# Kernel optimization log

Hardware: AMD Instinct MI355X
Metric: run time of the kernel (lower is better)

The kernel has to match this reference:

```python
import jax, jax.numpy as jnp
import numpy as np

PERMS = ((0, 1, 2, 3), (2, 1, 3, 0), (3, 1, 0, 2))


def setup_inputs() -> dict:
    key = jax.random.key(0)
    ks = jax.random.split(key, 10)
    N_n1, F = 50000, 128
    N_imp = 100000
    H = 512
    h = jax.random.normal(ks[0], (N_n1, F), dtype=jnp.float32)
    idx = jax.random.randint(ks[1], (N_imp, 4), 0, N_n1, dtype=jnp.int64)
    s = 0.05
    W1 = jax.random.normal(ks[2], (4 * F, H), dtype=jnp.float32) * s
    b1 = jax.random.normal(ks[3], (H,), dtype=jnp.float32) * s
    W2 = jax.random.normal(ks[4], (H, H), dtype=jnp.float32) * s
    b2 = jax.random.normal(ks[5], (H,), dtype=jnp.float32) * s
    W3 = jax.random.normal(ks[6], (H, H), dtype=jnp.float32) * s
    b3 = jax.random.normal(ks[7], (H,), dtype=jnp.float32) * s
    Wo = jax.random.normal(ks[8], (H, 2), dtype=jnp.float32) * s
    bo = jax.random.normal(ks[9], (2,), dtype=jnp.float32) * s
    return {"h": h, "idx": idx, "W1": W1, "b1": b1, "W2": W2, "b2": b2,
            "W3": W3, "b3": b3, "Wo": Wo, "bo": bo}


def reference(h, idx, W1, b1, W2, b2, W3, b3, Wo, bo):
    # Message passing: copy_u + mean over exactly one edge per relation == gather.
    hi = h[idx]  # [N, 4, F]
    N = hi.shape[0]
    # Stack the 3 permutations of the 4 neighbor features: [3, N, 4F]
    x = jnp.stack([hi[:, jnp.array(p), :].reshape(N, -1) for p in PERMS], axis=0)
    # Shared MLP (config = [512, relu] x 3), broadcast over permutation axis.
    x = jax.nn.relu(x @ W1 + b1)
    x = jax.nn.relu(x @ W2 + b2)
    x = jax.nn.relu(x @ W3 + b3)
    pooled = jnp.sum(x, axis=0)  # Janossy sum over permutations: [N, 512]
    return pooled @ Wo + bo  # [N, 2]
```

## Files before the change

### kernel.cpp

```cpp
#include <hip/hip_runtime.h>
#include <stdint.h>
#include <stddef.h>


typedef __attribute__((ext_vector_type(8))) short short8;
typedef __attribute__((ext_vector_type(16))) float f32x16;
typedef __attribute__((ext_vector_type(4))) float floatv4;
typedef __attribute__((ext_vector_type(8))) unsigned short ushort8;

#define GLOAD_LDS16(g, l)                                                      \
  __builtin_amdgcn_global_load_lds(                                            \
      (const __attribute__((address_space(1))) void*)(g),                      \
      (__attribute__((address_space(3))) void*)(l), 16, 0, 0)

__device__ __forceinline__ unsigned short f2bf(float f) {
  unsigned int u = __float_as_uint(f);
  u += 0x7fffu + ((u >> 16) & 1u);
  return (unsigned short)(u >> 16);
}
__device__ __forceinline__ float bf2f(unsigned short s) {
  return __uint_as_float(((unsigned int)s) << 16);
}

#define NNODES 100000
#define MTOT   300000
#define HD     512
#define NH     50000
#define LSTR   152

__global__ __launch_bounds__(256) void prep_w(const float* __restrict__ W1,
                                              const float* __restrict__ W2,
                                              const float* __restrict__ W3,
                                              unsigned short* __restrict__ Wt) {
  int t = blockIdx.x * 256 + threadIdx.x;
  int layer = t >> 18;
  int r = t & 262143;
  int e = r & 7;
  int q16 = r >> 3;
  int s = q16 & 1023;
  int blk = q16 >> 10;
  int nb = blk >> 3, kt = blk & 7;
  int c = ((s >> 8) << 1) | ((s >> 5) & 1);
  int row = ((s >> 6) & 3) * 32 + (s & 31);
  int n = nb * 128 + row;
  int k = kt * 64 + c * 8 + e;
  const float* W = layer == 0 ? W1 : (layer == 1 ? W2 : W3);
  Wt[t] = f2bf(W[k * 512 + n]);
}

__global__ __launch_bounds__(256) void prep_hb(const float* __restrict__ h,
                                               unsigned short* __restrict__ hb) {
  int t = blockIdx.x * 256 + threadIdx.x;
  int v = t >> 4, c8 = (t & 15) * 8;
  const floatv4* hp = (const floatv4*)(h + (size_t)v * 128 + c8);
  floatv4 f0 = hp[0], f1 = hp[1];
  ushort8 o;
#pragma unroll
  for (int e = 0; e < 4; ++e) {
    o[e] = f2bf(f0[e]);
    o[4 + e] = f2bf(f1[e]);
  }
  *(ushort8*)(hb + (size_t)v * 128 + c8) = o;
}

__global__ __launch_bounds__(256) void init_out(float* __restrict__ out,
                                                const float* __restrict__ bo) {
  int t = blockIdx.x * 256 + threadIdx.x;
  if (t < 2 * NNODES) out[t] = bo[t & 1];
}

template <int GATHER, int FINAL>
__global__ __launch_bounds__(256, 4) void gemm_k(
    const unsigned short* __restrict__ A,
    const int* __restrict__ idx,
    const unsigned short* __restrict__ Wt,
    const float* __restrict__ bias,
    unsigned short* __restrict__ Xout,
    float* __restrict__ out, const float* __restrict__ Wo,
    int mchunk0) {
  __shared__ __align__(16) char smem[39936];
  char* sA = smem;
  char* sB = smem + 16384;
  int* sIdx = (int*)(smem + 32768);
  float* sWo = (float*)(smem + 38912);

  const int t = threadIdx.x;
  int bx = blockIdx.x;
  int xcd = bx & 7, tq = bx >> 3;
  int cbk = tq & 3;
  int rb = xcd + ((tq >> 2) << 3);
  int n0 = cbk * 128;
  int rb8 = rb * 8;
  int w = t >> 6, l = t & 63;
  int wmq = (w >> 1) * 2, wnq = (w & 1) * 2;
  int m32 = l & 31, half = l >> 5;

  if (GATHER) {
    if (t < 128) {
      int m = mchunk0 + rb * 128 + t;
      unsigned um = (unsigned)m;
      unsigned n = um / 3u;
      int p = (int)(um - n * 3u);
      if (n >= NNODES) n = 0;
      const unsigned pk0 = 0x320u, pk1 = 0x111u, pk2 = 0x032u, pk3 = 0x203u;
      int sh = p * 4;
      sIdx[t * 4 + 0] = idx[n * 4 + ((pk0 >> sh) & 0xFu)];
      sIdx[t * 4 + 1] = idx[n * 4 + ((pk1 >> sh) & 0xFu)];
      sIdx[t * 4 + 2] = idx[n * 4 + ((pk2 >> sh) & 0xFu)];
      sIdx[t * 4 + 3] = idx[n * 4 + ((pk3 >> sh) & 0xFu)];
    }
    __syncthreads();
  }

  f32x16 acc[2][2];
#pragma unroll
  for (int i = 0; i < 2; ++i)
#pragma unroll
    for (int j = 0; j < 2; ++j)
#pragma unroll
      for (int r = 0; r < 16; ++r) acc[i][j][r] = 0.f;

  for (int kt = 0; kt < 8; ++kt) {
    if (GATHER) {
      int jn = kt >> 1;
      int base = (kt & 1) * 64;
      int row = ((t >> 6) & 3) * 32 + (t & 31);
      int src = sIdx[row * 4 + jn];
      int hbit = (t >> 5) & 1;
#pragma unroll
      for (int i = 0; i < 4; ++i) {
        int c = (i << 1) | hbit;
        GLOAD_LDS16(A + (size_t)src * 128 + base + c * 8,
                    sA + (i * 256 + t) * 16);
      }
    } else {
      const unsigned short* ga = A + ((size_t)(rb8 + kt) * 1024 + t) * 8;
#pragma unroll
      for (int i = 0; i < 4; ++i)
        GLOAD_LDS16(ga + (size_t)i * 2048, sA + (i * 256 + t) * 16);
    }
    {
      const unsigned short* gb = Wt + ((size_t)(cbk * 8 + kt) * 1024 + t) * 8;
#pragma unroll
      for (int i = 0; i < 4; ++i)
        GLOAD_LDS16(gb + (size_t)i * 2048, sB + (i * 256 + t) * 16);
    }
    __syncthreads();
#pragma unroll
    for (int ks = 0; ks < 4; ++ks) {
      short8 af[2], bfr[2];
#pragma unroll
      for (int i = 0; i < 2; ++i)
        af[i] = *(const short8*)(sA + (ks * 256 + (wmq + i) * 64 + l) * 16);
#pragma unroll
      for (int j = 0; j < 2; ++j)
        bfr[j] = *(const short8*)(sB + (ks * 256 + (wnq + j) * 64 + l) * 16);
#pragma unroll
      for (int i = 0; i < 2; ++i)
#pragma unroll
        for (int j = 0; j < 2; ++j)
          acc[i][j] = __builtin_amdgcn_mfma_f32_32x32x16_bf16(af[i], bfr[j],
                                                              acc[i][j], 0, 0, 0);
    }
    __syncthreads();
  }

  unsigned short* L = (unsigned short*)smem;
  if (FINAL && t < 256) sWo[t] = Wo[n0 * 2 + t];
#pragma unroll
  for (int i = 0; i < 2; ++i)
#pragma unroll
    for (int j = 0; j < 2; ++j) {
      int coll = wnq * 32 + j * 32 + m32;
      float bv = bias[n0 + coll];
#pragma unroll
      for (int r = 0; r < 16; ++r) {
        int rowl = wmq * 32 + i * 32 + (r & 3) + 8 * (r >> 2) + 4 * half;
        float v = fmaxf(acc[i][j][r] + bv, 0.f);
        L[rowl * LSTR + coll] = f2bf(v);
      }
    }
  __syncthreads();

  if (!FINAL) {
#pragma unroll
    for (int v = 0; v < 8; ++v) {
      int chunk = v * 256 + t;
      int ktsel = chunk >> 10;
      int s = chunk & 1023;
      int ks_l = s >> 8;
      int rowhi = (s >> 6) & 3;
      int hb_ = (s >> 5) & 1;
      int row = rowhi * 32 + (s & 31);
      int col_local = ktsel * 64 + (((ks_l << 1) | hb_) << 3);
      ushort8 val = *(const ushort8*)(L + row * LSTR + col_local);
      *(ushort8*)(Xout + ((size_t)(rb8 + 2 * cbk + ktsel) * 1024 + s) * 8) = val;
    }
  } else {
    int r2 = t >> 1, jo = t & 1;
    int grow = mchunk0 + rb * 128 + r2;
    if (grow < MTOT) {
      const unsigned short* Lr = L + r2 * LSTR;
      float s = 0.f;
#pragma unroll
      for (int cc = 0; cc < 128; cc += 2) {
        unsigned int pair = *(const unsigned int*)(Lr + cc);
        s += bf2f((unsigned short)(pair & 0xffffu)) * sWo[2 * cc + jo];
        s += bf2f((unsigned short)(pair >> 16)) * sWo[2 * cc + 2 + jo];
      }
      int node = grow / 3;
      atomicAdd(out + node * 2 + jo, s);
    }
  }
}

extern "C" void kernel_launch(void* const* d_in, const int* in_sizes, int n_in,
                              void* d_out, int out_size, void* d_ws,
                              size_t ws_size, hipStream_t stream) {
  const float* h  = (const float*)d_in[0];
  const int*   ix = (const int*)d_in[1];
  const float* W1 = (const float*)d_in[2];
  const float* b1 = (const float*)d_in[3];
  const float* W2 = (const float*)d_in[4];
  const float* b2 = (const float*)d_in[5];
  const float* W3 = (const float*)d_in[6];
  const float* b3 = (const float*)d_in[7];
  const float* Wo = (const float*)d_in[8];
  const float* bo = (const float*)d_in[9];
  float* out = (float*)d_out;

  unsigned short* ws = (unsigned short*)d_ws;
  unsigned short* Wt = ws;
  unsigned short* hb = Wt + 786432;
  unsigned short* bufs = hb + 6400000;
  const size_t baseBytes = (786432ull + 6400000ull) * 2;

  size_t avail = ws_size > baseBytes ? ws_size - baseBytes : 0;
  size_t ncap = avail / (2ull * 3 * HD * sizeof(unsigned short));
  size_t nc = (ncap / 2048) * 2048;
  if (nc > 32768) nc = 32768;
  if (nc == 0) nc = 2048;
  unsigned short* X1 = bufs;
  unsigned short* X2 = X1 + nc * 3 * HD;

  prep_w<<<3072, 256, 0, stream>>>(W1, W2, W3, Wt);
  prep_hb<<<NH * 16 / 256, 256, 0, stream>>>(h, hb);
  init_out<<<(2 * NNODES + 255) / 256, 256, 0, stream>>>(out, bo);

  for (size_t n0c = 0; n0c < NNODES; n0c += nc) {
    size_t remn = (size_t)NNODES - n0c;
    size_t ncp = remn < nc ? ((remn + 2047) / 2048) * 2048 : nc;
    int rows = (int)(ncp * 3);
    int RB = rows / 128;
    int m0 = (int)(3 * n0c);
    gemm_k<1, 0><<<RB * 4, 256, 0, stream>>>(hb, ix, Wt, b1, X1, nullptr,
                                             nullptr, m0);
    gemm_k<0, 0><<<RB * 4, 256, 0, stream>>>(X1, nullptr, Wt + 262144, b2, X2,
                                             nullptr, nullptr, m0);
    gemm_k<0, 1><<<RB * 4, 256, 0, stream>>>(X2, nullptr, Wt + 524288, b3,
                                             nullptr, out, Wo, m0);
  }
}
```

Before: 733.5 us.

## Load A fragments directly to registers and swizzle gathered A tile in LDS

For the non-gather layers, A tiles are already stored in MFMA fragment order, so each wave now reads its fragments straight from global memory into registers and skips the LDS staging for A. For the gather layer, gathered rows are laid out row-major in LDS with an XOR swizzle on the 16-byte column chunks, which makes each row's 128-byte read more contiguous in global memory and spreads LDS reads across banks. Together these aim to cut LDS traffic and make the gather loads more coalesced. The trade-off is more registers for the prefetched fragments, and global load latency now sits directly in front of the MFMAs.

```diff
diff --git a/kernel.cpp b/kernel.cpp
--- a/kernel.cpp
+++ b/kernel.cpp
@@ -79,8 +79,8 @@
     float* __restrict__ out, const float* __restrict__ Wo,
     int mchunk0) {
   __shared__ __align__(16) char smem[39936];
-  char* sA = smem;
-  char* sB = smem + 16384;
+  char* sB = smem;
+  char* sA = smem + 16384;
   int* sIdx = (int*)(smem + 32768);
   float* sWo = (float*)(smem + 38912);
 
@@ -94,6 +94,7 @@
   int w = t >> 6, l = t & 63;
   int wmq = (w >> 1) * 2, wnq = (w & 1) * 2;
   int m32 = l & 31, half = l >> 5;
+  int wm = wmq * 32;
 
   if (GATHER) {
     if (t < 128) {
@@ -121,23 +122,15 @@
       for (int r = 0; r < 16; ++r) acc[i][j][r] = 0.f;
 
   for (int kt = 0; kt < 8; ++kt) {
-    if (GATHER) {
-      int jn = kt >> 1;
-      int base = (kt & 1) * 64;
-      int row = ((t >> 6) & 3) * 32 + (t & 31);
-      int src = sIdx[row * 4 + jn];
-      int hbit = (t >> 5) & 1;
-#pragma unroll
-      for (int i = 0; i < 4; ++i) {
-        int c = (i << 1) | hbit;
-        GLOAD_LDS16(A + (size_t)src * 128 + base + c * 8,
-                    sA + (i * 256 + t) * 16);
-      }
-    } else {
-      const unsigned short* ga = A + ((size_t)(rb8 + kt) * 1024 + t) * 8;
-#pragma unroll
-      for (int i = 0; i < 4; ++i)
-        GLOAD_LDS16(ga + (size_t)i * 2048, sA + (i * 256 + t) * 16);
+    short8 afr[4][2];
+    if (!GATHER) {
+      const unsigned short* ga = A + ((size_t)(rb8 + kt) * 1024) * 8;
+#pragma unroll
+      for (int ks = 0; ks < 4; ++ks)
+#pragma unroll
+        for (int i = 0; i < 2; ++i)
+          afr[ks][i] = *(const short8*)(ga +
+              (size_t)(ks * 256 + (wmq + i) * 64 + l) * 8);
     }
     {
       const unsigned short* gb = Wt + ((size_t)(cbk * 8 + kt) * 1024 + t) * 8;
@@ -145,22 +138,45 @@
       for (int i = 0; i < 4; ++i)
         GLOAD_LDS16(gb + (size_t)i * 2048, sB + (i * 256 + t) * 16);
     }
+    if (GATHER) {
+      int jblk = kt >> 1;
+      int inner = (kt & 1) * 64;
+#pragma unroll
+      for (int i = 0; i < 4; ++i) {
+        int s = i * 256 + t;
+        int r = s >> 3;
+        int cl = (s & 7) ^ (r & 7);
+        int src = sIdx[r * 4 + jblk];
+        GLOAD_LDS16(A + (size_t)src * 128 + inner + cl * 8, sA + s * 16);
+      }
+    }
     __syncthreads();
 #pragma unroll
     for (int ks = 0; ks < 4; ++ks) {
-      short8 af[2], bfr[2];
-#pragma unroll
-      for (int i = 0; i < 2; ++i)
-        af[i] = *(const short8*)(sA + (ks * 256 + (wmq + i) * 64 + l) * 16);
+      short8 bfr[2];
 #pragma unroll
       for (int j = 0; j < 2; ++j)
         bfr[j] = *(const short8*)(sB + (ks * 256 + (wnq + j) * 64 + l) * 16);
-#pragma unroll
-      for (int i = 0; i < 2; ++i)
-#pragma unroll
-        for (int j = 0; j < 2; ++j)
-          acc[i][j] = __builtin_amdgcn_mfma_f32_32x32x16_bf16(af[i], bfr[j],
-                                                              acc[i][j], 0, 0, 0);
+      if (GATHER) {
+        short8 ag[2];
+        int cbp = ((ks << 1) + half) ^ (m32 & 7);
+#pragma unroll
+        for (int i = 0; i < 2; ++i)
+          ag[i] = *(const short8*)(sA + (wm + i * 32 + m32) * 128 + cbp * 16);
+#pragma unroll
+        for (int i = 0; i < 2; ++i)
+#pragma unroll
+          for (int j = 0; j < 2; ++j)
+            acc[i][j] = __builtin_amdgcn_mfma_f32_32x32x16_bf16(
+                ag[i], bfr[j], acc[i][j], 0, 0, 0);
+      } else {
+#pragma unroll
+        for (int i = 0; i < 2; ++i)
+#pragma unroll
+          for (int j = 0; j < 2; ++j)
+            acc[i][j] = __builtin_amdgcn_mfma_f32_32x32x16_bf16(
+                afr[ks][i], bfr[j], acc[i][j], 0, 0, 0);
+      }
     }
     __syncthreads();
   }
@@ -175,7 +191,7 @@
       float bv = bias[n0 + coll];
 #pragma unroll
       for (int r = 0; r < 16; ++r) {
-        int rowl = wmq * 32 + i * 32 + (r & 3) + 8 * (r >> 2) + 4 * half;
+        int rowl = wm + i * 32 + (r & 3) + 8 * (r >> 2) + 4 * half;
         float v = fmaxf(acc[i][j][r] + bv, 0.f);
         L[rowl * LSTR + coll] = f2bf(v);
       }
```

Result: faster. 652.9 us (-11.0%).
